# Kernel tuning notes

Measured on AMD Instinct MI355X. Metric: run time of the kernel, lower is better.

Reference implementation:

```python
import jax, jax.numpy as jnp
import numpy as np

SP = 4      # sp_size (number of simulated sequence-parallel ranks)
NH = 16     # num_attention_heads
HD = 64     # head_dim
HS = 1024   # hidden_size
B = 1       # batch
S = 8192    # global sequence length (SP chunks of 2048)


def setup_inputs() -> dict:
    key = jax.random.key(0)
    ks = jax.random.split(key, 9)
    w_scale = 1.0 / np.sqrt(HS)
    def w(k):
        # xavier-ish init, stored as [in, out] so y = x @ W + b
        return jax.random.uniform(k, (HS, HS), jnp.float32, -w_scale, w_scale)
    return {
        'hidden_states': jax.random.normal(ks[0], (B, S, HS), jnp.float32),
        'Wq': w(ks[1]), 'bq': jnp.zeros((HS,), jnp.float32),
        'Wk': w(ks[2]), 'bk': jnp.zeros((HS,), jnp.float32),
        'Wv': w(ks[3]), 'bv': jnp.zeros((HS,), jnp.float32),
        'Wo': w(ks[4]), 'bo': jnp.zeros((HS,), jnp.float32),
    }


def reference(hidden_states, Wq, bq, Wk, bk, Wv, bv, Wo, bo):
    b, s, _ = hidden_states.shape
    sc = s // SP  # per-rank chunk length
    inv_sqrt_hd = 1.0 / np.sqrt(HD)

    def heads(x):
        # [B, S, HS] -> [SP, B, NH, Sc, HD]
        return x.reshape(b, SP, sc, NH, HD).transpose(1, 0, 3, 2, 4)

    q = heads(hidden_states @ Wq + bq)
    k = heads(hidden_states @ Wk + bk)
    v = heads(hidden_states @ Wv + bv)

    out = jnp.zeros_like(q)
    # ring attention: at step i each rank r attends to chunk (r + i) mod SP
    for i in range(SP):
        ki = jnp.roll(k, -i, axis=0)
        vi = jnp.roll(v, -i, axis=0)
        scores = jnp.einsum('sbhqd,sbhkd->sbhqk', q, ki) * inv_sqrt_hd
        probs = jax.nn.softmax(scores, axis=-1)  # per-chunk softmax (faithful to source)
        out = out + jnp.einsum('sbhqk,sbhkd->sbhqd', probs, vi)
    out = out / SP  # source divides accumulated context by sp_size

    # [SP, B, NH, Sc, HD] -> [B, S, NH*HD]
    ctx = out.transpose(1, 0, 3, 2, 4).reshape(b, s, NH * HD)
    return ctx @ Wo + bo
```

## Files before the change

kernel.cpp:

```cpp
#include <hip/hip_runtime.h>

#define DEVINL __device__ __forceinline__

typedef __attribute__((ext_vector_type(8))) short short8;
typedef __attribute__((ext_vector_type(4))) float floatx4;
typedef __attribute__((ext_vector_type(2))) unsigned uintx2;

DEVINL unsigned short f2bf(float f){
  unsigned u = __builtin_bit_cast(unsigned, f);
  u += 0x7FFFu + ((u >> 16) & 1u);
  return (unsigned short)(u >> 16);
}
DEVINL unsigned pk2(float a, float b){
  unsigned ua = __builtin_bit_cast(unsigned, a);
  unsigned ub = __builtin_bit_cast(unsigned, b);
  ua += 0x7FFFu + ((ua >> 16) & 1u);
  ub += 0x7FFFu + ((ub >> 16) & 1u);
  return (ua >> 16) | (ub & 0xFFFF0000u);
}
DEVINL unsigned pkfast(float a, float b){
  unsigned ua = __builtin_bit_cast(unsigned, a) + 0x8000u;
  unsigned ub = __builtin_bit_cast(unsigned, b) + 0x8000u;
  return __builtin_amdgcn_perm(ub, ua, 0x07060302u);
}
DEVINL unsigned pkbf(float a, float b){
#if defined(__has_builtin)
#if __has_builtin(__builtin_amdgcn_cvt_pk_bf16_f32)
  typedef __attribute__((ext_vector_type(2))) __bf16 bf16x2_t;
  bf16x2_t r = __builtin_amdgcn_cvt_pk_bf16_f32(a, b);
  return __builtin_bit_cast(unsigned, r);
#else
  return pkfast(a, b);
#endif
#else
  return pkfast(a, b);
#endif
}
DEVINL float bf2f(unsigned short h){
  unsigned u = ((unsigned)h) << 16;
  return __builtin_bit_cast(float, u);
}
DEVINL void gload_lds16(const void* g, void* l){
  __builtin_amdgcn_global_load_lds((const __attribute__((address_space(1))) void*)g,
                                   (__attribute__((address_space(3))) void*)l, 16, 0, 0);
}
DEVINL int perm2(int k){
  return (((k >> 4) & 1) << 5) | (((k >> 2) & 3) << 3) | (((k >> 5) & 1) << 2) | (k & 3);
}

__global__ void k_detect(const unsigned* __restrict__ w, int* __restrict__ flag){
  __shared__ int cnt;
  if (threadIdx.x == 0) cnt = 0;
  __syncthreads();
  int c = 0;
  for (int i = threadIdx.x; i < 1024; i += 256){
    unsigned e = (w[i] >> 7) & 0xFFu;
    c += (e >= 120u && e <= 132u) ? 1 : 0;
  }
  atomicAdd(&cnt, c);
  __syncthreads();
  if (threadIdx.x == 0) *flag = (cnt > 512) ? 1 : 0;
}

__global__ void k_conv_bf16(const void* __restrict__ src, unsigned short* __restrict__ dst,
                            int n, const int* __restrict__ flag){
  int i = (blockIdx.x * 256 + threadIdx.x) * 8;
  if (i >= n) return;
  if (*flag){
    ((uint4*)dst)[i >> 3] = ((const uint4*)src)[i >> 3];
  } else {
    const float* s = (const float*)src;
    short8 v;
    #pragma unroll
    for (int j = 0; j < 8; j++) v[j] = (short)f2bf(s[i + j]);
    *(short8*)(dst + i) = v;
  }
}

__global__ void k_conv_wT4(const void* __restrict__ s0, const void* __restrict__ s1,
                           const void* __restrict__ s2, const void* __restrict__ s3,
                           unsigned short* __restrict__ d0, unsigned short* __restrict__ d1,
                           unsigned short* __restrict__ d2, unsigned short* __restrict__ d3,
                           const int* __restrict__ flag){
  __shared__ float tile[32][33];
  const void* src; unsigned short* dst;
  switch (blockIdx.z){
    case 0: src = s0; dst = d0; break;
    case 1: src = s1; dst = d1; break;
    case 2: src = s2; dst = d2; break;
    default: src = s3; dst = d3; break;
  }
  const int tx = threadIdx.x & 31, ty = threadIdx.x >> 5;
  const int bx = blockIdx.x, by = blockIdx.y;
  const int isbf = *flag;
  #pragma unroll
  for (int r = 0; r < 32; r += 8){
    int k = by*32 + ty + r, n = bx*32 + tx;
    float v = isbf ? bf2f(((const unsigned short*)src)[k*1024 + n])
                   : ((const float*)src)[k*1024 + n];
    tile[ty + r][tx] = v;
  }
  __syncthreads();
  #pragma unroll
  for (int r = 0; r < 32; r += 8){
    int n = bx*32 + ty + r, k = by*32 + tx;
    dst[n*1024 + k] = f2bf(tile[tx][ty + r]);
  }
}

__global__ void k_conv_b4(const void* __restrict__ s0, const void* __restrict__ s1,
                          const void* __restrict__ s2, const void* __restrict__ s3,
                          float* __restrict__ dst, const int* __restrict__ flag){
  int i = blockIdx.x * 256 + threadIdx.x;
  if (i >= 4096) return;
  int z = i >> 10, j = i & 1023;
  const void* s = (z == 0) ? s0 : (z == 1) ? s1 : (z == 2) ? s2 : s3;
  dst[i] = (*flag) ? bf2f(((const unsigned short*)s)[j]) : ((const float*)s)[j];
}

template<int MODE>
__global__ __launch_bounds__(256, 2) void k_gemm(
    const unsigned short* __restrict__ A, const unsigned short* __restrict__ Bt,
    const float* __restrict__ bias, void* __restrict__ C0, void* __restrict__ C1,
    void* __restrict__ C2, const int* __restrict__ flagp, float scale)
{
  const int K = 1024;
  __shared__ __align__(16) unsigned short As[128*32];
  __shared__ __align__(16) unsigned short Bs[128*32];
  const int tid = threadIdx.x;
  const int lane = tid & 63, wave = tid >> 6;
  const int quad = lane >> 4, l15 = lane & 15;
  const int m0 = blockIdx.x * 128, n0 = blockIdx.y * 128;
  const int wm = (wave >> 1) * 64, wn = (wave & 1) * 64;
  const floatx4 fzero = {0.f, 0.f, 0.f, 0.f};
  floatx4 acc[4][4];
  #pragma unroll
  for (int i = 0; i < 4; i++)
    #pragma unroll
    for (int j = 0; j < 4; j++) acc[i][j] = fzero;

  for (int k0 = 0; k0 < K; k0 += 32){
    __syncthreads();
    #pragma unroll
    for (int rep = 0; rep < 2; rep++){
      int idx = tid + rep*256;
      int row = idx >> 2, c = idx & 3;
      gload_lds16(A  + (size_t)(m0 + row)*K + (k0 + c*8), &As[idx*8]);
      gload_lds16(Bt + (size_t)(n0 + row)*K + (k0 + c*8), &Bs[idx*8]);
    }
    asm volatile("s_waitcnt vmcnt(0)" ::: "memory");
    __syncthreads();
    short8 af[4], bf[4];
    #pragma unroll
    for (int i = 0; i < 4; i++) af[i] = *(const short8*)&As[(wm + i*16 + l15)*32 + quad*8];
    #pragma unroll
    for (int j = 0; j < 4; j++) bf[j] = *(const short8*)&Bs[(wn + j*16 + l15)*32 + quad*8];
    #pragma unroll
    for (int i = 0; i < 4; i++)
      #pragma unroll
      for (int j = 0; j < 4; j++)
        acc[i][j] = __builtin_amdgcn_mfma_f32_16x16x32_bf16(af[i], bf[j], acc[i][j], 0, 0, 0);
  }

  float bs[4];
  #pragma unroll
  for (int j = 0; j < 4; j++) bs[j] = bias[n0 + wn + j*16 + l15];
  const int useBf = (MODE == 1) ? *flagp : 1;
  #pragma unroll
  for (int i = 0; i < 4; i++){
    #pragma unroll
    for (int j = 0; j < 4; j++){
      int n = n0 + wn + j*16 + l15;
      #pragma unroll
      for (int r = 0; r < 4; r++){
        int m = m0 + wm + i*16 + quad*4 + r;
        float v = acc[i][j][r] + bs[j];
        if (MODE == 3){
          int sel = n >> 10, nn = n & 1023;
          if (sel == 0){
            int dd = (nn & 63) ^ ((m & 7) << 3);
            ((unsigned short*)C0)[((size_t)(nn >> 6)*8192 + m)*64 + dd] = f2bf(v * scale);
          } else if (sel == 1){
            int dd = (nn & 63) ^ ((m & 7) << 3);
            ((unsigned short*)C1)[((size_t)(nn >> 6)*8192 + m)*64 + dd] = f2bf(v);
          } else {
            int s2 = perm2(m & 63) ^ ((nn & 7) << 3);
            ((unsigned short*)C2)[(size_t)nn*8192 + (m & ~63) + s2] = f2bf(v);
          }
        } else {
          if (useBf) ((unsigned short*)C0)[(size_t)m*1024 + n] = f2bf(v);
          else       ((float*)C0)[(size_t)m*1024 + n] = v;
        }
      }
    }
  }
}

template<int ATOMIC>
__global__ __launch_bounds__(512, 4) void k_attn(
    const unsigned short* __restrict__ Qg, const unsigned short* __restrict__ Kg,
    const unsigned short* __restrict__ Vg, float* __restrict__ outp)
{
  __shared__ __align__(16) unsigned short Qs[256*64];
  __shared__ __align__(16) unsigned short Ks[2][64*64];
  __shared__ __align__(16) unsigned short Vs[2][64*64];
  const int tid = threadIdx.x, lane = tid & 63, wave = tid >> 6;
  const int quad = lane >> 4, l15 = lane & 15;
  const int bid = blockIdx.x;
  const int xcd = bid & 7, slot = bid >> 3;
  const int h = xcd*2 + (slot >> 7);
  const int rem = slot & 127;
  const int rchunk = rem >> 5, rem2 = rem & 31;
  const int cidx = rem2 >> 3, qt = rem2 & 7;
  const int sq0 = rchunk*2048 + qt*256;
  const int kb = ((rchunk + cidx) & 3)*2048;
  const char* Qbase = (const char*)(Qg + (size_t)h*8192*64 + (size_t)sq0*64);
  const char* Kbase = (const char*)(Kg + (size_t)h*8192*64);
  const char* Vbase = (const char*)(Vg + (size_t)h*8192*64);
  const int wq0 = wave * 32;
  const floatx4 fz = {0.f, 0.f, 0.f, 0.f};

  const size_t voff = (size_t)(tid >> 3)*16384 + (size_t)(tid & 7)*16;
  auto stage = [&](int buf, int kvs){
    gload_lds16(Kbase + (size_t)kvs*128 + tid*16, (char*)Ks[buf] + tid*16);
    gload_lds16(Vbase + (size_t)kvs*2 + voff,     (char*)Vs[buf] + tid*16);
  };

  #pragma unroll
  for (int rep = 0; rep < 4; rep++){
    int idx = tid + rep*512;
    gload_lds16(Qbase + idx*16, (char*)Qs + idx*16);
  }
  stage(0, kb);
  asm volatile("s_waitcnt vmcnt(0)" ::: "memory");
  __syncthreads();

  short8 qf[2][2];
  #pragma unroll
  for (int mi = 0; mi < 2; mi++)
    #pragma unroll
    for (int ks = 0; ks < 2; ks++){
      int row = wq0 + mi*16 + l15;
      qf[mi][ks] = *(const short8*)&Qs[row*64 + (((ks*4 + quad) ^ (row & 7)))*8];
    }

  short8 ones;
  #pragma unroll
  for (int j = 0; j < 8; j++) ones[j] = (short)0x3F80;

  floatx4 Oc[2][4], Ol[2];
  #pragma unroll
  for (int mi = 0; mi < 2; mi++){
    Ol[mi] = fz;
    #pragma unroll
    for (int di = 0; di < 4; di++) Oc[mi][di] = fz;
  }

  for (int kt = 0; kt < 32; kt++){
    const int cur = kt & 1;
    asm volatile("s_waitcnt vmcnt(0)" ::: "memory");
    __syncthreads();
    if (kt < 31) stage(cur ^ 1, kb + (kt + 1)*64);

    short8 pf[2][2];
    #pragma unroll
    for (int mi = 0; mi < 2; mi++){
      floatx4 St[4];
      #pragma unroll
      for (int ni = 0; ni < 4; ni++){
        int krow = ni*16 + l15;
        short8 kf = *(const short8*)&Ks[cur][krow*64 + ((quad ^ (krow & 7)))*8];
        St[ni] = __builtin_amdgcn_mfma_f32_16x16x32_bf16(kf, qf[mi][0], fz, 0, 0, 0);
      }
      #pragma unroll
      for (int ni = 0; ni < 4; ni++){
        int krow = ni*16 + l15;
        short8 kf = *(const short8*)&Ks[cur][krow*64 + (((4 + quad) ^ (krow & 7)))*8];
        St[ni] = __builtin_amdgcn_mfma_f32_16x16x32_bf16(kf, qf[mi][1], St[ni], 0, 0, 0);
      }
      #pragma unroll
      for (int ni = 0; ni < 4; ni++)
        #pragma unroll
        for (int r = 0; r < 4; r++)
          St[ni][r] = __builtin_amdgcn_exp2f(St[ni][r]);
      #pragma unroll
      for (int ks = 0; ks < 2; ks++){
        uintx2 lo, hi;
        lo[0] = pkbf(St[ks  ][0], St[ks  ][1]);
        lo[1] = pkbf(St[ks  ][2], St[ks  ][3]);
        hi[0] = pkbf(St[2+ks][0], St[2+ks][1]);
        hi[1] = pkbf(St[2+ks][2], St[2+ks][3]);
        union { uintx2 u[2]; short8 s; } cv;
        cv.u[0] = lo; cv.u[1] = hi;
        pf[mi][ks] = cv.s;
      }
    }

    #pragma unroll
    for (int ks = 0; ks < 2; ks++){
      #pragma unroll
      for (int di = 0; di < 4; di++){
        int vrow = di*16 + l15;
        short8 vf = *(const short8*)&Vs[cur][vrow*64 + (((ks*4 + quad) ^ (vrow & 7)))*8];
        #pragma unroll
        for (int mi = 0; mi < 2; mi++)
          Oc[mi][di] = __builtin_amdgcn_mfma_f32_16x16x32_bf16(vf, pf[mi][ks], Oc[mi][di], 0, 0, 0);
      }
      #pragma unroll
      for (int mi = 0; mi < 2; mi++)
        Ol[mi] = __builtin_amdgcn_mfma_f32_16x16x32_bf16(ones, pf[mi][ks], Ol[mi], 0, 0, 0);
    }
  }

  #pragma unroll
  for (int mi = 0; mi < 2; mi++){
    float inv = __builtin_amdgcn_rcpf(Ol[mi][0]) * 0.25f;
    int q = sq0 + wq0 + mi*16 + l15;
    #pragma unroll
    for (int di = 0; di < 4; di++){
      size_t addr = (size_t)q*1024 + h*64 + di*16 + quad*4;
      if (ATOMIC){
        #pragma unroll
        for (int r = 0; r < 4; r++) atomicAdd(&outp[addr + r], Oc[mi][di][r] * inv);
      } else {
        floatx4 v;
        #pragma unroll
        for (int r = 0; r < 4; r++) v[r] = Oc[mi][di][r] * inv;
        *(floatx4*)&outp[(size_t)cidx*8192*1024 + addr] = v;
      }
    }
  }
}

__global__ void k_redux4(const float* __restrict__ part, unsigned short* __restrict__ ctx){
  const size_t P = (size_t)8192*1024;
  size_t i = ((size_t)blockIdx.x * 256 + threadIdx.x) * 4;
  if (i >= P) return;
  floatx4 a = *(const floatx4*)&part[i];
  floatx4 b = *(const floatx4*)&part[P + i];
  floatx4 c = *(const floatx4*)&part[2*P + i];
  floatx4 d = *(const floatx4*)&part[3*P + i];
  uintx2 w;
  w[0] = pk2(a[0]+b[0]+c[0]+d[0], a[1]+b[1]+c[1]+d[1]);
  w[1] = pk2(a[2]+b[2]+c[2]+d[2], a[3]+b[3]+c[3]+d[3]);
  *(uintx2*)&ctx[i] = w;
}

__global__ void k_cvt1(const float* __restrict__ acc, unsigned short* __restrict__ ctx){
  const size_t P = (size_t)8192*1024;
  size_t i = ((size_t)blockIdx.x * 256 + threadIdx.x) * 4;
  if (i >= P) return;
  floatx4 a = *(const floatx4*)&acc[i];
  uintx2 w;
  w[0] = pk2(a[0], a[1]);
  w[1] = pk2(a[2], a[3]);
  *(uintx2*)&ctx[i] = w;
}

__global__ void k_zero(float* __restrict__ p){
  const size_t P = (size_t)8192*1024;
  size_t i = ((size_t)blockIdx.x * 256 + threadIdx.x) * 4;
  if (i >= P) return;
  floatx4 z = {0.f, 0.f, 0.f, 0.f};
  *(floatx4*)&p[i] = z;
}

extern "C" void kernel_launch(void* const* d_in, const int* in_sizes, int n_in,
                              void* d_out, int out_size, void* d_ws, size_t ws_size,
                              hipStream_t stream)
{
  (void)in_sizes; (void)n_in; (void)out_size;
  char* ws = (char*)d_ws;
  size_t off = 0;
  auto alloc = [&](size_t bytes) -> char* {
    char* p = ws + off;
    off = (off + bytes + 255) & ~(size_t)255;
    return p;
  };
  int* flag            = (int*)alloc(4);
  float* biasAll       = (float*)alloc(4096*4);
  unsigned short* wqt  = (unsigned short*)alloc((size_t)1024*1024*2);
  unsigned short* wkt  = (unsigned short*)alloc((size_t)1024*1024*2);
  unsigned short* wvt  = (unsigned short*)alloc((size_t)1024*1024*2);
  unsigned short* wot  = (unsigned short*)alloc((size_t)1024*1024*2);
  unsigned short* hsb  = (unsigned short*)alloc((size_t)8192*1024*2);
  unsigned short* Qb   = (unsigned short*)alloc((size_t)16*8192*64*2);
  unsigned short* Kb   = (unsigned short*)alloc((size_t)16*8192*64*2);
  unsigned short* Vb   = (unsigned short*)alloc((size_t)16*8192*64*2);
  unsigned short* ctxb = hsb;
  size_t base = off;
  const size_t PLANE = (size_t)8192*1024*4;
  const bool planes_fit = (ws_size >= base + 4*PLANE);

  k_detect<<<1, 256, 0, stream>>>((const unsigned*)d_in[0], flag);
  k_conv_bf16<<<4096, 256, 0, stream>>>(d_in[0], hsb, 8192*1024, flag);
  k_conv_wT4<<<dim3(32,32,4), 256, 0, stream>>>(d_in[1], d_in[3], d_in[5], d_in[7],
                                                wqt, wkt, wvt, wot, flag);
  k_conv_b4<<<16, 256, 0, stream>>>(d_in[2], d_in[4], d_in[6], d_in[8], biasAll, flag);

  const float Cs = 0.18033688011112042f;
  k_gemm<3><<<dim3(64, 24), 256, 0, stream>>>(hsb, wqt, biasAll, Qb, Kb, Vb, nullptr, Cs);

  if (planes_fit){
    float* part = (float*)(ws + base);
    k_attn<0><<<2048, 512, 0, stream>>>(Qb, Kb, Vb, part);
    k_redux4<<<8192, 256, 0, stream>>>(part, ctxb);
  } else {
    float* ctxf = (float*)(ws + base);
    k_zero<<<8192, 256, 0, stream>>>(ctxf);
    k_attn<1><<<2048, 512, 0, stream>>>(Qb, Kb, Vb, ctxf);
    k_cvt1<<<8192, 256, 0, stream>>>(ctxf, ctxb);
  }

  k_gemm<1><<<dim3(64, 8), 256, 0, stream>>>(ctxb, wot, biasAll + 3072, d_out,
                                             nullptr, nullptr, flag, 1.0f);
}
```

Before: 487.7 us.

## Software-pipeline attention with triple-buffered KV and smaller 128-row query tiles

The attention kernel moves from 512-thread blocks with 256 query rows to 256-thread blocks with 128 rows, doubling the grid. Q fragments are now loaded straight from global memory into registers instead of through LDS. K/V staging becomes triple-buffered, two tiles ahead, and the loop is software-pipelined so the QK^T/exp of tile t+1 overlaps the PV MFMAs of tile t, with a prologue and epilogue. This aims to hide LDS and MFMA latency, at the cost of more registers for the doubled P buffers and more K/V reloads per query row.

```diff
diff --git a/kernel.cpp b/kernel.cpp
--- a/kernel.cpp
+++ b/kernel.cpp
@@ -197,52 +197,52 @@
 }
 
 template<int ATOMIC>
-__global__ __launch_bounds__(512, 4) void k_attn(
+__global__ __launch_bounds__(256, 3) void k_attn(
     const unsigned short* __restrict__ Qg, const unsigned short* __restrict__ Kg,
     const unsigned short* __restrict__ Vg, float* __restrict__ outp)
 {
-  __shared__ __align__(16) unsigned short Qs[256*64];
-  __shared__ __align__(16) unsigned short Ks[2][64*64];
-  __shared__ __align__(16) unsigned short Vs[2][64*64];
+  __shared__ __align__(16) unsigned short Ks[3][64*64];
+  __shared__ __align__(16) unsigned short Vs[3][64*64];
   const int tid = threadIdx.x, lane = tid & 63, wave = tid >> 6;
   const int quad = lane >> 4, l15 = lane & 15;
   const int bid = blockIdx.x;
   const int xcd = bid & 7, slot = bid >> 3;
-  const int h = xcd*2 + (slot >> 7);
-  const int rem = slot & 127;
-  const int rchunk = rem >> 5, rem2 = rem & 31;
-  const int cidx = rem2 >> 3, qt = rem2 & 7;
-  const int sq0 = rchunk*2048 + qt*256;
+  const int h = xcd*2 + (slot >> 8);
+  const int rem = slot & 255;
+  const int rchunk = rem >> 6, rem2 = rem & 63;
+  const int cidx = rem2 >> 4, qt = rem2 & 15;
+  const int sq0 = rchunk*2048 + qt*128;
   const int kb = ((rchunk + cidx) & 3)*2048;
-  const char* Qbase = (const char*)(Qg + (size_t)h*8192*64 + (size_t)sq0*64);
+  const unsigned short* Qh = Qg + (size_t)h*8192*64;
   const char* Kbase = (const char*)(Kg + (size_t)h*8192*64);
   const char* Vbase = (const char*)(Vg + (size_t)h*8192*64);
   const int wq0 = wave * 32;
   const floatx4 fz = {0.f, 0.f, 0.f, 0.f};
 
-  const size_t voff = (size_t)(tid >> 3)*16384 + (size_t)(tid & 7)*16;
+  const int idx0 = tid, idx1 = tid + 256;
+  const size_t voff0 = (size_t)(idx0 >> 3)*16384 + (idx0 & 7)*16;
+  const size_t voff1 = (size_t)(idx1 >> 3)*16384 + (idx1 & 7)*16;
   auto stage = [&](int buf, int kvs){
-    gload_lds16(Kbase + (size_t)kvs*128 + tid*16, (char*)Ks[buf] + tid*16);
-    gload_lds16(Vbase + (size_t)kvs*2 + voff,     (char*)Vs[buf] + tid*16);
+    const char* Kt = Kbase + (size_t)kvs*128;
+    const char* Vt = Vbase + (size_t)kvs*2;
+    gload_lds16(Kt + idx0*16, (char*)Ks[buf] + idx0*16);
+    gload_lds16(Kt + idx1*16, (char*)Ks[buf] + idx1*16);
+    gload_lds16(Vt + voff0, (char*)Vs[buf] + idx0*16);
+    gload_lds16(Vt + voff1, (char*)Vs[buf] + idx1*16);
   };
 
-  #pragma unroll
-  for (int rep = 0; rep < 4; rep++){
-    int idx = tid + rep*512;
-    gload_lds16(Qbase + idx*16, (char*)Qs + idx*16);
-  }
+  short8 qf[2][2];
+  #pragma unroll
+  for (int mi = 0; mi < 2; mi++)
+    #pragma unroll
+    for (int ks = 0; ks < 2; ks++){
+      int row = sq0 + wq0 + mi*16 + l15;
+      qf[mi][ks] = *(const short8*)(Qh + (size_t)row*64 + (((ks*4 + quad) ^ (row & 7)))*8);
+    }
   stage(0, kb);
-  asm volatile("s_waitcnt vmcnt(0)" ::: "memory");
+  stage(1, kb + 64);
+  asm volatile("s_waitcnt vmcnt(4)" ::: "memory");
   __syncthreads();
-
-  short8 qf[2][2];
-  #pragma unroll
-  for (int mi = 0; mi < 2; mi++)
-    #pragma unroll
-    for (int ks = 0; ks < 2; ks++){
-      int row = wq0 + mi*16 + l15;
-      qf[mi][ks] = *(const short8*)&Qs[row*64 + (((ks*4 + quad) ^ (row & 7)))*8];
-    }
 
   short8 ones;
   #pragma unroll
@@ -256,26 +256,62 @@
     for (int di = 0; di < 4; di++) Oc[mi][di] = fz;
   }
 
-  for (int kt = 0; kt < 32; kt++){
-    const int cur = kt & 1;
+  short8 P[2][2][2];
+
+  #pragma unroll
+  for (int mi = 0; mi < 2; mi++){
+    floatx4 St[4];
+    #pragma unroll
+    for (int ni = 0; ni < 4; ni++){
+      int krow = ni*16 + l15;
+      short8 kf = *(const short8*)&Ks[0][krow*64 + ((quad ^ (krow & 7)))*8];
+      St[ni] = __builtin_amdgcn_mfma_f32_16x16x32_bf16(kf, qf[mi][0], fz, 0, 0, 0);
+    }
+    #pragma unroll
+    for (int ni = 0; ni < 4; ni++){
+      int krow = ni*16 + l15;
+      short8 kf = *(const short8*)&Ks[0][krow*64 + (((4 + quad) ^ (krow & 7)))*8];
+      St[ni] = __builtin_amdgcn_mfma_f32_16x16x32_bf16(kf, qf[mi][1], St[ni], 0, 0, 0);
+    }
+    #pragma unroll
+    for (int ni = 0; ni < 4; ni++)
+      #pragma unroll
+      for (int r = 0; r < 4; r++)
+        St[ni][r] = __builtin_amdgcn_exp2f(St[ni][r]);
+    #pragma unroll
+    for (int ks = 0; ks < 2; ks++){
+      uintx2 lo, hi;
+      lo[0] = pkbf(St[ks  ][0], St[ks  ][1]);
+      lo[1] = pkbf(St[ks  ][2], St[ks  ][3]);
+      hi[0] = pkbf(St[2+ks][0], St[2+ks][1]);
+      hi[1] = pkbf(St[2+ks][2], St[2+ks][3]);
+      union { uintx2 u[2]; short8 s; } cv;
+      cv.u[0] = lo; cv.u[1] = hi;
+      P[0][mi][ks] = cv.s;
+    }
+  }
+
+  #pragma unroll
+  for (int t = 0; t < 31; t++){
+    const int cur = t % 3, nb1 = (t + 1) % 3, nb2 = (t + 2) % 3;
+    const int pc = t & 1, pn = pc ^ 1;
     asm volatile("s_waitcnt vmcnt(0)" ::: "memory");
     __syncthreads();
-    if (kt < 31) stage(cur ^ 1, kb + (kt + 1)*64);
-
-    short8 pf[2][2];
+    if (t < 30) stage(nb2, kb + (t + 2)*64);
+
     #pragma unroll
     for (int mi = 0; mi < 2; mi++){
       floatx4 St[4];
       #pragma unroll
       for (int ni = 0; ni < 4; ni++){
         int krow = ni*16 + l15;
-        short8 kf = *(const short8*)&Ks[cur][krow*64 + ((quad ^ (krow & 7)))*8];
+        short8 kf = *(const short8*)&Ks[nb1][krow*64 + ((quad ^ (krow & 7)))*8];
         St[ni] = __builtin_amdgcn_mfma_f32_16x16x32_bf16(kf, qf[mi][0], fz, 0, 0, 0);
       }
       #pragma unroll
       for (int ni = 0; ni < 4; ni++){
         int krow = ni*16 + l15;
-        short8 kf = *(const short8*)&Ks[cur][krow*64 + (((4 + quad) ^ (krow & 7)))*8];
+        short8 kf = *(const short8*)&Ks[nb1][krow*64 + (((4 + quad) ^ (krow & 7)))*8];
         St[ni] = __builtin_amdgcn_mfma_f32_16x16x32_bf16(kf, qf[mi][1], St[ni], 0, 0, 0);
       }
       #pragma unroll
@@ -292,7 +328,7 @@
         hi[1] = pkbf(St[2+ks][2], St[2+ks][3]);
         union { uintx2 u[2]; short8 s; } cv;
         cv.u[0] = lo; cv.u[1] = hi;
-        pf[mi][ks] = cv.s;
+        P[pn][mi][ks] = cv.s;
       }
     }
 
@@ -304,12 +340,27 @@
         short8 vf = *(const short8*)&Vs[cur][vrow*64 + (((ks*4 + quad) ^ (vrow & 7)))*8];
         #pragma unroll
         for (int mi = 0; mi < 2; mi++)
-          Oc[mi][di] = __builtin_amdgcn_mfma_f32_16x16x32_bf16(vf, pf[mi][ks], Oc[mi][di], 0, 0, 0);
+          Oc[mi][di] = __builtin_amdgcn_mfma_f32_16x16x32_bf16(vf, P[pc][mi][ks], Oc[mi][di], 0, 0, 0);
       }
       #pragma unroll
       for (int mi = 0; mi < 2; mi++)
-        Ol[mi] = __builtin_amdgcn_mfma_f32_16x16x32_bf16(ones, pf[mi][ks], Ol[mi], 0, 0, 0);
-    }
+        Ol[mi] = __builtin_amdgcn_mfma_f32_16x16x32_bf16(ones, P[pc][mi][ks], Ol[mi], 0, 0, 0);
+    }
+  }
+
+  #pragma unroll
+  for (int ks = 0; ks < 2; ks++){
+    #pragma unroll
+    for (int di = 0; di < 4; di++){
+      int vrow = di*16 + l15;
+      short8 vf = *(const short8*)&Vs[31 % 3][vrow*64 + (((ks*4 + quad) ^ (vrow & 7)))*8];
+      #pragma unroll
+      for (int mi = 0; mi < 2; mi++)
+        Oc[mi][di] = __builtin_amdgcn_mfma_f32_16x16x32_bf16(vf, P[1][mi][ks], Oc[mi][di], 0, 0, 0);
+    }
+    #pragma unroll
+    for (int mi = 0; mi < 2; mi++)
+      Ol[mi] = __builtin_amdgcn_mfma_f32_16x16x32_bf16(ones, P[1][mi][ks], Ol[mi], 0, 0, 0);
   }
 
   #pragma unroll
@@ -403,12 +454,12 @@
 
   if (planes_fit){
     float* part = (float*)(ws + base);
-    k_attn<0><<<2048, 512, 0, stream>>>(Qb, Kb, Vb, part);
+    k_attn<0><<<4096, 256, 0, stream>>>(Qb, Kb, Vb, part);
     k_redux4<<<8192, 256, 0, stream>>>(part, ctxb);
   } else {
     float* ctxf = (float*)(ws + base);
     k_zero<<<8192, 256, 0, stream>>>(ctxf);
-    k_attn<1><<<2048, 512, 0, stream>>>(Qb, Kb, Vb, ctxf);
+    k_attn<1><<<4096, 256, 0, stream>>>(Qb, Kb, Vb, ctxf);
     k_cvt1<<<8192, 256, 0, stream>>>(ctxf, ctxb);
   }
 
```

Result: slower. 503.3 us (+3.2%).
